# Kernel tuning notes

Hardware: AMD Instinct MI355X
Metric: run time of the kernel (lower is better)

The kernel has to match this reference:

```python
import jax, jax.numpy as jnp
import numpy as np

B, L, DEPTH, W = 32, 256, 4, 32

def setup_inputs() -> dict:
    key = jax.random.key(0)
    ks = jax.random.split(key, 12)
    rn = lambda k, sh: jax.random.normal(k, sh, dtype=jnp.float32)
    return {
        "x": rn(ks[0], (B, L, L)),
        "ai": rn(ks[1], (W, 1)),
        "ao": rn(ks[2], (1, W)),
        "a": rn(ks[3], (DEPTH, W, W)),
        "bi": rn(ks[4], (W, 1)),
        "bo": rn(ks[5], (1, W)),
        "b": rn(ks[6], (DEPTH, W, W)),
        "ci": rn(ks[7], (W, 1)),
        "co": rn(ks[8], (1, W)),
        "c": rn(ks[9], (DEPTH, W, W)),
        "bias_i": rn(ks[10], (W,)),
        "bias": rn(ks[11], (DEPTH, W)),
    }

def _layer(x, wc, wb, wa, bias):
    # x: [b, ci, X, Y]; wc/wb/wa: [co, ci]; circular 3x3 stencil via rolls
    y = jnp.einsum('oi,bixy->boxy', wc, x)
    nb = (jnp.roll(x, 1, axis=2) + jnp.roll(x, -1, axis=2)
          + jnp.roll(x, 1, axis=3) + jnp.roll(x, -1, axis=3))
    y = y + jnp.einsum('oi,bixy->boxy', wb, nb)
    dg = (jnp.roll(x, (1, 1), axis=(2, 3)) + jnp.roll(x, (-1, -1), axis=(2, 3))
          + jnp.roll(x, (1, -1), axis=(2, 3)) + jnp.roll(x, (-1, 1), axis=(2, 3)))
    y = y + jnp.einsum('oi,bixy->boxy', wa, dg)
    if bias is not None:
        y = y + bias[None, :, None, None]
    return y

def _act(x):
    # torch nn.GELU() default is exact (erf-based)
    return jax.nn.gelu(x, approximate=False)

def _func(x, ai, ao, a, bi, bo, b, ci, co, c, bias_i, bias):
    h = x[:, None, :, :]                       # [b,1,L,L]
    h = _act(_layer(h, ci, bi, ai, bias_i))    # [b,W,L,L]
    for k in range(a.shape[0]):
        h = _act(_layer(h, c[k], b[k], a[k], bias[k]))
    y = _layer(h, co, bo, ao, None)            # [b,1,L,L]
    return jnp.squeeze(y, axis=1)              # [b,L,L]

def reference(x, ai, ao, a, bi, bo, b, ci, co, c, bias_i, bias):
    f = lambda v: _func(v, ai, ao, a, bi, bo, b, ci, co, c, bias_i, bias)
    return 0.5 * (f(x) - f(-x))
```

## Files before the change

### kernel.cpp

```cpp
#include <hip/hip_runtime.h>
#include <hip/hip_bf16.h>

#define B_ 32
#define L_ 256
#define W_ 32
#define TILE 16
#define PSTR 40
#define LL (L_*L_)

typedef float    floatx4 __attribute__((ext_vector_type(4)));
typedef float    floatx2 __attribute__((ext_vector_type(2)));
typedef short    shortx8 __attribute__((ext_vector_type(8)));
typedef unsigned uintx2  __attribute__((ext_vector_type(2)));
typedef unsigned uintx4  __attribute__((ext_vector_type(4)));

typedef const __attribute__((address_space(1))) unsigned guint_t;
typedef __attribute__((address_space(3))) unsigned luint_t;

__device__ __forceinline__ void lds_dma16(const unsigned short* src, unsigned short* dst) {
    __builtin_amdgcn_global_load_lds((guint_t*)src, (luint_t*)dst, 16, 0, 0);
}

__device__ __forceinline__ floatx2 fma2(floatx2 a, floatx2 b, floatx2 c) {
#if __has_builtin(__builtin_elementwise_fma)
    return __builtin_elementwise_fma(a, b, c);
#else
    return floatx2{fmaf(a.x, b.x, c.x), fmaf(a.y, b.y, c.y)};
#endif
}

#if __has_builtin(__builtin_amdgcn_cvt_pk_bf16_f32)
__device__ __forceinline__ unsigned pack_bf2(float a, float b) {
    auto v = __builtin_amdgcn_cvt_pk_bf16_f32(a, b);
    return __builtin_bit_cast(unsigned, v);
}
#else
__device__ __forceinline__ unsigned pack_bf2(float a, float b) {
    unsigned ua = __float_as_uint(a);
    unsigned ub = __float_as_uint(b);
    ua += 0x7fffu + ((ua >> 16) & 1u);
    ub += 0x7fffu + ((ub >> 16) & 1u);
    return (ua >> 16) | (ub & 0xffff0000u);
}
#endif

__device__ __forceinline__ unsigned gelu2_pack(floatx2 x) {
    floatx2 x2    = x * x;
    floatx2 t     = x2 * 0.044715f;
    floatx2 inner = fma2(t, x, x);
    floatx2 z     = inner * -2.3022082299446597f;
    float e0 = __builtin_amdgcn_exp2f(z.x);
    float e1 = __builtin_amdgcn_exp2f(z.y);
    float r0 = __builtin_amdgcn_rcpf(1.0f + e0);
    float r1 = __builtin_amdgcn_rcpf(1.0f + e1);
    floatx2 g = x * floatx2{r0, r1};
    return pack_bf2(g.x, g.y);
}

__device__ __forceinline__ int swizzle_blk(int p) {
    return (p & 7) * 1024 + (p >> 3);
}

__device__ __forceinline__ void conv9(
        const shortx8& t00, const shortx8& t01, const shortx8& t02,
        const shortx8& t10, const shortx8& t11, const shortx8& t12,
        const shortx8& t20, const shortx8& t21, const shortx8& t22,
        const shortx8 af[3][2], const floatx4 bvv[2], floatx4 acc[2]) {
    #pragma unroll
    for (int h = 0; h < 2; ++h) {
        acc[h] = __builtin_amdgcn_mfma_f32_16x16x32_bf16(af[0][h], t11, bvv[h], 0, 0, 0);
        acc[h] = __builtin_amdgcn_mfma_f32_16x16x32_bf16(af[1][h], t01, acc[h], 0, 0, 0);
        acc[h] = __builtin_amdgcn_mfma_f32_16x16x32_bf16(af[1][h], t21, acc[h], 0, 0, 0);
        acc[h] = __builtin_amdgcn_mfma_f32_16x16x32_bf16(af[1][h], t10, acc[h], 0, 0, 0);
        acc[h] = __builtin_amdgcn_mfma_f32_16x16x32_bf16(af[1][h], t12, acc[h], 0, 0, 0);
        acc[h] = __builtin_amdgcn_mfma_f32_16x16x32_bf16(af[2][h], t00, acc[h], 0, 0, 0);
        acc[h] = __builtin_amdgcn_mfma_f32_16x16x32_bf16(af[2][h], t02, acc[h], 0, 0, 0);
        acc[h] = __builtin_amdgcn_mfma_f32_16x16x32_bf16(af[2][h], t20, acc[h], 0, 0, 0);
        acc[h] = __builtin_amdgcn_mfma_f32_16x16x32_bf16(af[2][h], t22, acc[h], 0, 0, 0);
    }
}

__device__ __forceinline__ void conv9x2(
        const shortx8 r0[3], const shortx8 r1[3],
        const shortx8 r2[3], const shortx8 r3[3],
        const shortx8 af[3][2], const floatx4 bvv[2],
        floatx4 accA[2], floatx4 accB[2]) {
    const shortx8* ra[3] = { r0, r1, r2 };
    const shortx8* rb[3] = { r1, r2, r3 };
    const int F[9] = {0,1,1,1,1,2,2,2,2};
    const int R[9] = {1,0,2,1,1,0,0,2,2};
    const int C[9] = {1,1,1,0,2,0,2,0,2};
    #pragma unroll
    for (int k = 0; k < 9; ++k)
      #pragma unroll
      for (int h = 0; h < 2; ++h) {
        accA[h] = __builtin_amdgcn_mfma_f32_16x16x32_bf16(af[F[k]][h], ra[R[k]][C[k]],
                      (k == 0) ? bvv[h] : accA[h], 0, 0, 0);
        accB[h] = __builtin_amdgcn_mfma_f32_16x16x32_bf16(af[F[k]][h], rb[R[k]][C[k]],
                      (k == 0) ? bvv[h] : accB[h], 0, 0, 0);
      }
}

__device__ __forceinline__ void conv9x2_last(
        const shortx8 r0[3], const shortx8 r1[3],
        const shortx8 r2[3], const shortx8 r3[3],
        const shortx8 afl[3], const floatx4& zc, floatx4& accA, floatx4& accB) {
    const shortx8* ra[3] = { r0, r1, r2 };
    const shortx8* rb[3] = { r1, r2, r3 };
    const int F[9] = {0,1,1,1,1,2,2,2,2};
    const int R[9] = {1,0,2,1,1,0,0,2,2};
    const int C[9] = {1,1,1,0,2,0,2,0,2};
    #pragma unroll
    for (int k = 0; k < 9; ++k) {
        accA = __builtin_amdgcn_mfma_f32_16x16x32_bf16(afl[F[k]], ra[R[k]][C[k]],
                   (k == 0) ? zc : accA, 0, 0, 0);
        accB = __builtin_amdgcn_mfma_f32_16x16x32_bf16(afl[F[k]], rb[R[k]][C[k]],
                   (k == 0) ? zc : accB, 0, 0, 0);
    }
}

__device__ __forceinline__ void gelu_pack4(const floatx4 acc[2], unsigned d[4]) {
    d[0] = gelu2_pack(floatx2{acc[0][0], acc[0][1]});
    d[1] = gelu2_pack(floatx2{acc[0][2], acc[0][3]});
    d[2] = gelu2_pack(floatx2{acc[1][0], acc[1][1]});
    d[3] = gelu2_pack(floatx2{acc[1][2], acc[1][3]});
}

__device__ __forceinline__ void build_afrag(
        const float* wc, const float* wb, const float* wa, const float* bias,
        int m, int q, shortx8 af[3][2], floatx4 bvv[2]) {
    const float* wm[3] = { wc, wb, wa };
    #pragma unroll
    for (int f = 0; f < 3; ++f)
      #pragma unroll
      for (int h = 0; h < 2; ++h) {
        const float* row = wm[f] + (h*16 + m) * W_ + q*8;
        floatx4 r0 = *(const floatx4*)(row);
        floatx4 r1 = *(const floatx4*)(row + 4);
        union { shortx8 s; unsigned u[4]; } w;
        w.u[0] = pack_bf2(r0.x, r0.y);
        w.u[1] = pack_bf2(r0.z, r0.w);
        w.u[2] = pack_bf2(r1.x, r1.y);
        w.u[3] = pack_bf2(r1.z, r1.w);
        af[f][h] = w.s;
      }
    #pragma unroll
    for (int h = 0; h < 2; ++h)
        bvv[h] = *(const floatx4*)(bias + h*16 + q*4);
}

__global__ __launch_bounds__(256) void kern_first(
        const float* __restrict__ x, float scale,
        const float* __restrict__ ci, const float* __restrict__ bi,
        const float* __restrict__ ai, const float* __restrict__ bias_i,
        unsigned short* __restrict__ hout) {
    __shared__ float tile[18*18];
    __shared__ float wC[W_], wB[W_], wA[W_], bs[W_];
    int blk = swizzle_blk(blockIdx.x);
    int b = blk >> 8;
    int t = blk & 255;
    int x0 = (t >> 4) * TILE;
    int y0 = (t & 15) * TILE;
    int tid = threadIdx.x;
    if (tid < W_) { wC[tid] = ci[tid]; wB[tid] = bi[tid]; wA[tid] = ai[tid]; bs[tid] = bias_i[tid]; }
    const float* xb = x + (size_t)b * LL;
    for (int idx = tid; idx < 18*18; idx += 256) {
        int dy = idx / 18, dx = idx % 18;
        int gx = (x0 + dy - 1) & 255;
        int gy = (y0 + dx - 1) & 255;
        tile[idx] = scale * xb[gx * L_ + gy];
    }
    __syncthreads();
    int dx = tid & 15, dy = tid >> 4;
    const float* c0 = &tile[dy * 18 + dx];
    float ctr = c0[19];
    float nb  = c0[1] + c0[37] + c0[18] + c0[20];
    float dg  = c0[0] + c0[2] + c0[36] + c0[38];
    floatx2 ctr2 = floatx2{ctr, ctr};
    floatx2 nb2  = floatx2{nb, nb};
    floatx2 dg2  = floatx2{dg, dg};
    unsigned od[16];
    #pragma unroll
    for (int o = 0; o < 16; ++o) {
        floatx2 wcv = *(const floatx2*)(&wC[2*o]);
        floatx2 wbv = *(const floatx2*)(&wB[2*o]);
        floatx2 wav = *(const floatx2*)(&wA[2*o]);
        floatx2 bsv = *(const floatx2*)(&bs[2*o]);
        floatx2 v = fma2(wcv, ctr2, fma2(wbv, nb2, fma2(wav, dg2, bsv)));
        od[o] = gelu2_pack(v);
    }
    unsigned* dst = (unsigned*)(hout + (((((size_t)b << 8) | (unsigned)(x0+dy)) << 8 | (unsigned)(y0+dx)) << 5));
    *(uintx4*)(dst)      = uintx4{od[0],  od[1],  od[2],  od[3]};
    *(uintx4*)(dst + 4)  = uintx4{od[4],  od[5],  od[6],  od[7]};
    *(uintx4*)(dst + 8)  = uintx4{od[8],  od[9],  od[10], od[11]};
    *(uintx4*)(dst + 12) = uintx4{od[12], od[13], od[14], od[15]};
}

__global__ __launch_bounds__(256, 4) void kern_mid2(
        const unsigned short* __restrict__ hin,
        const float* __restrict__ wc1, const float* __restrict__ wb1,
        const float* __restrict__ wa1, const float* __restrict__ bias1,
        const float* __restrict__ wc2, const float* __restrict__ wb2,
        const float* __restrict__ wa2, const float* __restrict__ bias2,
        unsigned short* __restrict__ hout) {
    __shared__ unsigned short tile2[400 * PSTR];

    const int tid = threadIdx.x;
    const int blk = swizzle_blk(blockIdx.x);
    const int b  = blk >> 8;
    const int t  = blk & 255;
    const int x0 = (t >> 4) * TILE;
    const int y0 = (t & 15) * TILE;

    const unsigned short* hb = hin + ((size_t)b << 21);

    #pragma unroll
    for (int jj = 0; jj < 8; ++jj) {
        int j = tid + jj * 256;
        if (j < 2000) {
            int pos = (j * 3277) >> 14;
            int qtr = j - pos * 5;
            int qe  = qtr < 4 ? qtr : 3;
            int r = (pos * 3277) >> 16;
            int c = pos - r * 20;
            int gx = (x0 + r - 2) & 255;
            int gy = (y0 + c - 2) & 255;
            const unsigned short* src = hb + ((((unsigned)gx << 8) | (unsigned)gy) << 5) + qe*8;
            lds_dma16(src, tile2 + (size_t)j * 8);
        }
    }

    const int lane = tid & 63;
    const int wv   = tid >> 6;
    const int m    = lane & 15;
    const int q    = lane >> 4;

    shortx8 afrag[3][2];
    floatx4 bvv[2];
    build_afrag(wc1, wb1, wa1, bias1, m, q, afrag, bvv);

    __syncthreads();

#define LDT(tr, off) (*(const shortx8*)(tile2 + (((tr)*20 + m + (off)))*PSTR + q*8))

    const int trow0 = wv * 4;
    shortx8 R0[3], R1[3], R2[3], R3[3], R4[3], R5[3];
    #pragma unroll
    for (int o = 0; o < 3; ++o) {
        R0[o] = LDT(trow0 + 0, o);
        R1[o] = LDT(trow0 + 1, o);
        R2[o] = LDT(trow0 + 2, o);
        R3[o] = LDT(trow0 + 3, o);
    }
    unsigned heldA[2][4];
    {
        floatx4 accA[2], accB[2];
        conv9x2(R0, R1, R2, R3, afrag, bvv, accA, accB);
        gelu_pack4(accA, heldA[0]);
        gelu_pack4(accB, heldA[1]);
    }
    #pragma unroll
    for (int o = 0; o < 3; ++o) {
        R4[o] = LDT(trow0 + 4, o);
        R5[o] = LDT(trow0 + 5, o);
    }
    {
        floatx4 accA[2], accB[2];
        conv9x2(R2, R3, R4, R5, afrag, bvv, accA, accB);
        unsigned dA[4], dB[4];
        gelu_pack4(accA, dA);
        gelu_pack4(accB, dB);
        unsigned short* wpA = tile2 + ((trow0 + 2)*20 + m)*PSTR + q*4;
        *(uintx2*)(wpA)      = uintx2{dA[0], dA[1]};
        *(uintx2*)(wpA + 16) = uintx2{dA[2], dA[3]};
        unsigned short* wpB = tile2 + ((trow0 + 3)*20 + m)*PSTR + q*4;
        *(uintx2*)(wpB)      = uintx2{dB[0], dB[1]};
        *(uintx2*)(wpB + 16) = uintx2{dB[2], dB[3]};
    }

    int er0, ec0;
    if (wv == 0)      { er0 = 16; ec0 = m;  }
    else if (wv == 1) { er0 = 17; ec0 = m;  }
    else if (wv == 2) { er0 = m;  ec0 = 16; }
    else              { er0 = m;  ec0 = 17; }
    unsigned heldE[4];
    {
        shortx8 T[3][3];
        #pragma unroll
        for (int i = 0; i < 3; ++i)
          #pragma unroll
          for (int o = 0; o < 3; ++o)
            T[i][o] = *(const shortx8*)(tile2 + ((er0 + i)*20 + ec0 + o)*PSTR + q*8);
        floatx4 acc[2];
        conv9(T[0][0], T[0][1], T[0][2], T[1][0], T[1][1], T[1][2],
              T[2][0], T[2][1], T[2][2], afrag, bvv, acc);
        gelu_pack4(acc, heldE);
    }
    const int heldEoff = (er0*20 + ec0)*PSTR + q*4;

    unsigned heldC[4];
    int heldCoff = 0;
    if (wv == 2) {
        int sr = 16 + ((m >> 1) & 1);
        int sc = 16 + (m & 1);
        shortx8 T[3][3];
        #pragma unroll
        for (int i = 0; i < 3; ++i)
          #pragma unroll
          for (int o = 0; o < 3; ++o)
            T[i][o] = *(const shortx8*)(tile2 + ((sr + i)*20 + sc + o)*PSTR + q*8);
        floatx4 acc[2];
        conv9(T[0][0], T[0][1], T[0][2], T[1][0], T[1][1], T[1][2],
              T[2][0], T[2][1], T[2][2], afrag, bvv, acc);
        gelu_pack4(acc, heldC);
        heldCoff = (sr*20 + sc)*PSTR + q*4;
    }

    __syncthreads();

    #pragma unroll
    for (int rr = 0; rr < 2; ++rr) {
        unsigned short* wp = tile2 + ((trow0 + rr)*20 + m)*PSTR + q*4;
        *(uintx2*)(wp)      = uintx2{heldA[rr][0], heldA[rr][1]};
        *(uintx2*)(wp + 16) = uintx2{heldA[rr][2], heldA[rr][3]};
    }
    {
        unsigned short* wp = tile2 + heldEoff;
        *(uintx2*)(wp)      = uintx2{heldE[0], heldE[1]};
        *(uintx2*)(wp + 16) = uintx2{heldE[2], heldE[3]};
    }
    if (wv == 2 && m < 4) {
        unsigned short* wp = tile2 + heldCoff;
        *(uintx2*)(wp)      = uintx2{heldC[0], heldC[1]};
        *(uintx2*)(wp + 16) = uintx2{heldC[2], heldC[3]};
    }

    build_afrag(wc2, wb2, wa2, bias2, m, q, afrag, bvv);

    __syncthreads();

    unsigned short* outb = hout + ((size_t)b << 21);
    #pragma unroll
    for (int o = 0; o < 3; ++o) {
        R0[o] = LDT(trow0 + 0, o);
        R1[o] = LDT(trow0 + 1, o);
        R2[o] = LDT(trow0 + 2, o);
        R3[o] = LDT(trow0 + 3, o);
    }
    {
        floatx4 accA[2], accB[2];
        conv9x2(R0, R1, R2, R3, afrag, bvv, accA, accB);
        unsigned dA[4], dB[4];
        gelu_pack4(accA, dA);
        gelu_pack4(accB, dB);
        unsigned short* dstA = outb + ((((unsigned)(x0 + trow0 + 0) << 8) | (unsigned)(y0 + m)) << 5) + q*4;
        *(uintx2*)(dstA)      = uintx2{dA[0], dA[1]};
        *(uintx2*)(dstA + 16) = uintx2{dA[2], dA[3]};
        unsigned short* dstB = outb + ((((unsigned)(x0 + trow0 + 1) << 8) | (unsigned)(y0 + m)) << 5) + q*4;
        *(uintx2*)(dstB)      = uintx2{dB[0], dB[1]};
        *(uintx2*)(dstB + 16) = uintx2{dB[2], dB[3]};
    }
    #pragma unroll
    for (int o = 0; o < 3; ++o) {
        R4[o] = LDT(trow0 + 4, o);
        R5[o] = LDT(trow0 + 5, o);
    }
    {
        floatx4 accA[2], accB[2];
        conv9x2(R2, R3, R4, R5, afrag, bvv, accA, accB);
        unsigned dA[4], dB[4];
        gelu_pack4(accA, dA);
        gelu_pack4(accB, dB);
        unsigned short* dstA = outb + ((((unsigned)(x0 + trow0 + 2) << 8) | (unsigned)(y0 + m)) << 5) + q*4;
        *(uintx2*)(dstA)      = uintx2{dA[0], dA[1]};
        *(uintx2*)(dstA + 16) = uintx2{dA[2], dA[3]};
        unsigned short* dstB = outb + ((((unsigned)(x0 + trow0 + 3) << 8) | (unsigned)(y0 + m)) << 5) + q*4;
        *(uintx2*)(dstB)      = uintx2{dB[0], dB[1]};
        *(uintx2*)(dstB + 16) = uintx2{dB[2], dB[3]};
    }
#undef LDT
}

__global__ __launch_bounds__(256, 6) void kern_last(
        const unsigned short* __restrict__ hin,
        const float* __restrict__ co, const float* __restrict__ bo,
        const float* __restrict__ ao,
        float* __restrict__ out, int mode) {
    __shared__ unsigned short tile2[324 * PSTR];
    const int tid = threadIdx.x;
    const int blk = swizzle_blk(blockIdx.x);
    const int b  = blk >> 8;
    const int t  = blk & 255;
    const int x0 = (t >> 4) * TILE;
    const int y0 = (t & 15) * TILE;

    const unsigned short* hb = hin + ((size_t)b << 21);
    #pragma unroll
    for (int jj = 0; jj < 7; ++jj) {
        int j = tid + jj * 256;
        if (j < 1620) {
            int pos = (j * 3277) >> 14;
            int qtr = j - pos * 5;
            int qe  = qtr < 4 ? qtr : 3;
            int r = (pos * 3641) >> 16;
            int c = pos - r * 18;
            int gx = (x0 + r - 1) & 255;
            int gy = (y0 + c - 1) & 255;
            const unsigned short* src = hb + ((((unsigned)gx << 8) | (unsigned)gy) << 5) + qe*8;
            lds_dma16(src, tile2 + (size_t)j * 8);
        }
    }

    const int lane = tid & 63;
    const int wv   = tid >> 6;
    const int m    = lane & 15;
    const int q    = lane >> 4;

    const float* wm[3] = { co, bo, ao };
    shortx8 afl[3];
    float z = (m == 0) ? 1.0f : 0.0f;
    #pragma unroll
    for (int f = 0; f < 3; ++f) {
        const float* row = wm[f] + q*8;
        floatx4 r0 = *(const floatx4*)(row);
        floatx4 r1 = *(const floatx4*)(row + 4);
        union { shortx8 s; unsigned u[4]; } w;
        w.u[0] = pack_bf2(r0.x * z, r0.y * z);
        w.u[1] = pack_bf2(r0.z * z, r0.w * z);
        w.u[2] = pack_bf2(r1.x * z, r1.y * z);
        w.u[3] = pack_bf2(r1.z * z, r1.w * z);
        afl[f] = w.s;
    }
    const floatx4 zc = {0.f, 0.f, 0.f, 0.f};

    __syncthreads();

#define LDT18(tr, off) (*(const shortx8*)(tile2 + (((tr)*18 + m + (off)))*PSTR + q*8))
    const int trow0 = wv * 4;
    shortx8 R0[3], R1[3], R2[3], R3[3], R4[3], R5[3];
    #pragma unroll
    for (int o = 0; o < 3; ++o) {
        R0[o] = LDT18(trow0 + 0, o);
        R1[o] = LDT18(trow0 + 1, o);
        R2[o] = LDT18(trow0 + 2, o);
        R3[o] = LDT18(trow0 + 3, o);
    }
    {
        floatx4 aA, aB;
        conv9x2_last(R0, R1, R2, R3, afl, zc, aA, aB);
        if (q == 0) {
            size_t o0 = (size_t)b * LL + (size_t)(x0 + trow0 + 0) * L_ + (y0 + m);
            size_t o1 = (size_t)b * LL + (size_t)(x0 + trow0 + 1) * L_ + (y0 + m);
            float v0 = 0.5f * aA[0];
            float v1 = 0.5f * aB[0];
            if (mode == 0) { out[o0] = v0;           out[o1] = v1;           }
            else           { out[o0] = out[o0] - v0; out[o1] = out[o1] - v1; }
        }
    }
    #pragma unroll
    for (int o = 0; o < 3; ++o) {
        R4[o] = LDT18(trow0 + 4, o);
        R5[o] = LDT18(trow0 + 5, o);
    }
    {
        floatx4 aA, aB;
        conv9x2_last(R2, R3, R4, R5, afl, zc, aA, aB);
        if (q == 0) {
            size_t o0 = (size_t)b * LL + (size_t)(x0 + trow0 + 2) * L_ + (y0 + m);
            size_t o1 = (size_t)b * LL + (size_t)(x0 + trow0 + 3) * L_ + (y0 + m);
            float v0 = 0.5f * aA[0];
            float v1 = 0.5f * aB[0];
            if (mode == 0) { out[o0] = v0;           out[o1] = v1;           }
            else           { out[o0] = out[o0] - v0; out[o1] = out[o1] - v1; }
        }
    }
#undef LDT18
}

extern "C" void kernel_launch(void* const* d_in, const int* in_sizes, int n_in,
                              void* d_out, int out_size, void* d_ws, size_t ws_size,
                              hipStream_t stream) {
    const float* x      = (const float*)d_in[0];
    const float* ai     = (const float*)d_in[1];
    const float* ao     = (const float*)d_in[2];
    const float* a      = (const float*)d_in[3];
    const float* bi     = (const float*)d_in[4];
    const float* bo     = (const float*)d_in[5];
    const float* b      = (const float*)d_in[6];
    const float* ci     = (const float*)d_in[7];
    const float* co     = (const float*)d_in[8];
    const float* c      = (const float*)d_in[9];
    const float* bias_i = (const float*)d_in[10];
    const float* bias   = (const float*)d_in[11];
    float* out = (float*)d_out;

    const size_t elems = (size_t)B_ * W_ * LL;
    unsigned short* hA = (unsigned short*)d_ws;
    unsigned short* hB = hA + elems;

    dim3 grid(B_ * 256), blk(256);
    const int WW = W_ * W_;
    for (int s = 0; s < 2; ++s) {
        float scale = s ? -1.0f : 1.0f;
        kern_first<<<grid, blk, 0, stream>>>(x, scale, ci, bi, ai, bias_i, hA);
        kern_mid2<<<grid, blk, 0, stream>>>(hA,
            c, b, a, bias,
            c + WW, b + WW, a + WW, bias + W_,
            hB);
        kern_mid2<<<grid, blk, 0, stream>>>(hB,
            c + 2*WW, b + 2*WW, a + 2*WW, bias + 2*W_,
            c + 3*WW, b + 3*WW, a + 3*WW, bias + 3*W_,
            hA);
        kern_last<<<grid, blk, 0, stream>>>(hA, co, bo, ao, out, s);
    }
}
```

Baseline: 721.0 us.

## Fuse first pointwise layer with the first two stencil layers in one kernel

The first 1-channel stencil layer is now computed inside a new fused kernel that builds a 20x20 halo tile of layer-0 activations in LDS from a 22x22 input patch, then runs two MFMA stencil layers as kern_mid2 did. This removes one full-size bf16 activation write and read through global memory and one kernel launch per sign pass. In exchange each block recomputes the halo ring of layer 0 and uses more LDS, which may reduce occupancy.

```diff
diff --git a/kernel.cpp b/kernel.cpp
--- a/kernel.cpp
+++ b/kernel.cpp
@@ -7,6 +7,7 @@
 #define TILE 16
 #define PSTR 40
 #define LL (L_*L_)
+#define ELEMS ((size_t)B_ * W_ * LL)
 
 typedef float    floatx4 __attribute__((ext_vector_type(4)));
 typedef float    floatx2 __attribute__((ext_vector_type(2)));
@@ -43,6 +44,13 @@
     return (ua >> 16) | (ub & 0xffff0000u);
 }
 #endif
+
+__device__ __forceinline__ float gelu_fast(float x) {
+    float x2 = x * x;
+    float inner = fmaf(0.044715f * x2, x, x);
+    float e = __builtin_amdgcn_exp2f(inner * -2.3022082299446597f);
+    return x * __builtin_amdgcn_rcpf(1.0f + e);
+}
 
 __device__ __forceinline__ unsigned gelu2_pack(floatx2 x) {
     floatx2 x2    = x * x;
@@ -61,14 +69,15 @@
     return (p & 7) * 1024 + (p >> 3);
 }
 
-__device__ __forceinline__ void conv9(
+__device__ __forceinline__ void conv9_v1(
         const shortx8& t00, const shortx8& t01, const shortx8& t02,
         const shortx8& t10, const shortx8& t11, const shortx8& t12,
         const shortx8& t20, const shortx8& t21, const shortx8& t22,
-        const shortx8 af[3][2], const floatx4 bvv[2], floatx4 acc[2]) {
+        const shortx8 af[3][2], const float bv[2][4], floatx4 acc[2]) {
     #pragma unroll
     for (int h = 0; h < 2; ++h) {
-        acc[h] = __builtin_amdgcn_mfma_f32_16x16x32_bf16(af[0][h], t11, bvv[h], 0, 0, 0);
+        acc[h] = floatx4{bv[h][0], bv[h][1], bv[h][2], bv[h][3]};
+        acc[h] = __builtin_amdgcn_mfma_f32_16x16x32_bf16(af[0][h], t11, acc[h], 0, 0, 0);
         acc[h] = __builtin_amdgcn_mfma_f32_16x16x32_bf16(af[1][h], t01, acc[h], 0, 0, 0);
         acc[h] = __builtin_amdgcn_mfma_f32_16x16x32_bf16(af[1][h], t21, acc[h], 0, 0, 0);
         acc[h] = __builtin_amdgcn_mfma_f32_16x16x32_bf16(af[1][h], t10, acc[h], 0, 0, 0);
@@ -80,55 +89,16 @@
     }
 }
 
-__device__ __forceinline__ void conv9x2(
-        const shortx8 r0[3], const shortx8 r1[3],
-        const shortx8 r2[3], const shortx8 r3[3],
-        const shortx8 af[3][2], const floatx4 bvv[2],
-        floatx4 accA[2], floatx4 accB[2]) {
-    const shortx8* ra[3] = { r0, r1, r2 };
-    const shortx8* rb[3] = { r1, r2, r3 };
-    const int F[9] = {0,1,1,1,1,2,2,2,2};
-    const int R[9] = {1,0,2,1,1,0,0,2,2};
-    const int C[9] = {1,1,1,0,2,0,2,0,2};
-    #pragma unroll
-    for (int k = 0; k < 9; ++k)
-      #pragma unroll
-      for (int h = 0; h < 2; ++h) {
-        accA[h] = __builtin_amdgcn_mfma_f32_16x16x32_bf16(af[F[k]][h], ra[R[k]][C[k]],
-                      (k == 0) ? bvv[h] : accA[h], 0, 0, 0);
-        accB[h] = __builtin_amdgcn_mfma_f32_16x16x32_bf16(af[F[k]][h], rb[R[k]][C[k]],
-                      (k == 0) ? bvv[h] : accB[h], 0, 0, 0);
-      }
-}
-
-__device__ __forceinline__ void conv9x2_last(
-        const shortx8 r0[3], const shortx8 r1[3],
-        const shortx8 r2[3], const shortx8 r3[3],
-        const shortx8 afl[3], const floatx4& zc, floatx4& accA, floatx4& accB) {
-    const shortx8* ra[3] = { r0, r1, r2 };
-    const shortx8* rb[3] = { r1, r2, r3 };
-    const int F[9] = {0,1,1,1,1,2,2,2,2};
-    const int R[9] = {1,0,2,1,1,0,0,2,2};
-    const int C[9] = {1,1,1,0,2,0,2,0,2};
-    #pragma unroll
-    for (int k = 0; k < 9; ++k) {
-        accA = __builtin_amdgcn_mfma_f32_16x16x32_bf16(afl[F[k]], ra[R[k]][C[k]],
-                   (k == 0) ? zc : accA, 0, 0, 0);
-        accB = __builtin_amdgcn_mfma_f32_16x16x32_bf16(afl[F[k]], rb[R[k]][C[k]],
-                   (k == 0) ? zc : accB, 0, 0, 0);
-    }
-}
-
-__device__ __forceinline__ void gelu_pack4(const floatx4 acc[2], unsigned d[4]) {
-    d[0] = gelu2_pack(floatx2{acc[0][0], acc[0][1]});
-    d[1] = gelu2_pack(floatx2{acc[0][2], acc[0][3]});
-    d[2] = gelu2_pack(floatx2{acc[1][0], acc[1][1]});
-    d[3] = gelu2_pack(floatx2{acc[1][2], acc[1][3]});
-}
-
-__device__ __forceinline__ void build_afrag(
+__device__ __forceinline__ void gelu_pack4_v1(const floatx4 acc[2], unsigned d[4]) {
+    d[0] = pack_bf2(gelu_fast(acc[0][0]), gelu_fast(acc[0][1]));
+    d[1] = pack_bf2(gelu_fast(acc[0][2]), gelu_fast(acc[0][3]));
+    d[2] = pack_bf2(gelu_fast(acc[1][0]), gelu_fast(acc[1][1]));
+    d[3] = pack_bf2(gelu_fast(acc[1][2]), gelu_fast(acc[1][3]));
+}
+
+__device__ __forceinline__ void build_afrag_v1(
         const float* wc, const float* wb, const float* wa, const float* bias,
-        int m, int q, shortx8 af[3][2], floatx4 bvv[2]) {
+        int m, int q, shortx8 af[3][2], float bv[2][4]) {
     const float* wm[3] = { wc, wb, wa };
     #pragma unroll
     for (int f = 0; f < 3; ++f)
@@ -146,54 +116,293 @@
       }
     #pragma unroll
     for (int h = 0; h < 2; ++h)
+      #pragma unroll
+      for (int r = 0; r < 4; ++r)
+        bv[h][r] = bias[h*16 + q*4 + r];
+}
+
+__device__ __forceinline__ void conv9(
+        const shortx8& t00, const shortx8& t01, const shortx8& t02,
+        const shortx8& t10, const shortx8& t11, const shortx8& t12,
+        const shortx8& t20, const shortx8& t21, const shortx8& t22,
+        const shortx8 af[3][2], const floatx4 bvv[2], floatx4 acc[2]) {
+    #pragma unroll
+    for (int h = 0; h < 2; ++h) {
+        acc[h] = __builtin_amdgcn_mfma_f32_16x16x32_bf16(af[0][h], t11, bvv[h], 0, 0, 0);
+        acc[h] = __builtin_amdgcn_mfma_f32_16x16x32_bf16(af[1][h], t01, acc[h], 0, 0, 0);
+        acc[h] = __builtin_amdgcn_mfma_f32_16x16x32_bf16(af[1][h], t21, acc[h], 0, 0, 0);
+        acc[h] = __builtin_amdgcn_mfma_f32_16x16x32_bf16(af[1][h], t10, acc[h], 0, 0, 0);
+        acc[h] = __builtin_amdgcn_mfma_f32_16x16x32_bf16(af[1][h], t12, acc[h], 0, 0, 0);
+        acc[h] = __builtin_amdgcn_mfma_f32_16x16x32_bf16(af[2][h], t00, acc[h], 0, 0, 0);
+        acc[h] = __builtin_amdgcn_mfma_f32_16x16x32_bf16(af[2][h], t02, acc[h], 0, 0, 0);
+        acc[h] = __builtin_amdgcn_mfma_f32_16x16x32_bf16(af[2][h], t20, acc[h], 0, 0, 0);
+        acc[h] = __builtin_amdgcn_mfma_f32_16x16x32_bf16(af[2][h], t22, acc[h], 0, 0, 0);
+    }
+}
+
+__device__ __forceinline__ void conv9x2(
+        const shortx8 r0[3], const shortx8 r1[3],
+        const shortx8 r2[3], const shortx8 r3[3],
+        const shortx8 af[3][2], const floatx4 bvv[2],
+        floatx4 accA[2], floatx4 accB[2]) {
+    const shortx8* ra[3] = { r0, r1, r2 };
+    const shortx8* rb[3] = { r1, r2, r3 };
+    const int F[9] = {0,1,1,1,1,2,2,2,2};
+    const int R[9] = {1,0,2,1,1,0,0,2,2};
+    const int C[9] = {1,1,1,0,2,0,2,0,2};
+    #pragma unroll
+    for (int k = 0; k < 9; ++k)
+      #pragma unroll
+      for (int h = 0; h < 2; ++h) {
+        accA[h] = __builtin_amdgcn_mfma_f32_16x16x32_bf16(af[F[k]][h], ra[R[k]][C[k]],
+                      (k == 0) ? bvv[h] : accA[h], 0, 0, 0);
+        accB[h] = __builtin_amdgcn_mfma_f32_16x16x32_bf16(af[F[k]][h], rb[R[k]][C[k]],
+                      (k == 0) ? bvv[h] : accB[h], 0, 0, 0);
+      }
+}
+
+__device__ __forceinline__ void conv9x2_last(
+        const shortx8 r0[3], const shortx8 r1[3],
+        const shortx8 r2[3], const shortx8 r3[3],
+        const shortx8 afl[3], const floatx4& zc, floatx4& accA, floatx4& accB) {
+    const shortx8* ra[3] = { r0, r1, r2 };
+    const shortx8* rb[3] = { r1, r2, r3 };
+    const int F[9] = {0,1,1,1,1,2,2,2,2};
+    const int R[9] = {1,0,2,1,1,0,0,2,2};
+    const int C[9] = {1,1,1,0,2,0,2,0,2};
+    #pragma unroll
+    for (int k = 0; k < 9; ++k) {
+        accA = __builtin_amdgcn_mfma_f32_16x16x32_bf16(afl[F[k]], ra[R[k]][C[k]],
+                   (k == 0) ? zc : accA, 0, 0, 0);
+        accB = __builtin_amdgcn_mfma_f32_16x16x32_bf16(afl[F[k]], rb[R[k]][C[k]],
+                   (k == 0) ? zc : accB, 0, 0, 0);
+    }
+}
+
+__device__ __forceinline__ void gelu_pack4(const floatx4 acc[2], unsigned d[4]) {
+    d[0] = gelu2_pack(floatx2{acc[0][0], acc[0][1]});
+    d[1] = gelu2_pack(floatx2{acc[0][2], acc[0][3]});
+    d[2] = gelu2_pack(floatx2{acc[1][0], acc[1][1]});
+    d[3] = gelu2_pack(floatx2{acc[1][2], acc[1][3]});
+}
+
+__device__ __forceinline__ void build_afrag(
+        const float* wc, const float* wb, const float* wa, const float* bias,
+        int m, int q, shortx8 af[3][2], floatx4 bvv[2]) {
+    const float* wm[3] = { wc, wb, wa };
+    #pragma unroll
+    for (int f = 0; f < 3; ++f)
+      #pragma unroll
+      for (int h = 0; h < 2; ++h) {
+        const float* row = wm[f] + (h*16 + m) * W_ + q*8;
+        floatx4 r0 = *(const floatx4*)(row);
+        floatx4 r1 = *(const floatx4*)(row + 4);
+        union { shortx8 s; unsigned u[4]; } w;
+        w.u[0] = pack_bf2(r0.x, r0.y);
+        w.u[1] = pack_bf2(r0.z, r0.w);
+        w.u[2] = pack_bf2(r1.x, r1.y);
+        w.u[3] = pack_bf2(r1.z, r1.w);
+        af[f][h] = w.s;
+      }
+    #pragma unroll
+    for (int h = 0; h < 2; ++h)
         bvv[h] = *(const floatx4*)(bias + h*16 + q*4);
 }
 
-__global__ __launch_bounds__(256) void kern_first(
+__global__ __launch_bounds__(256, 4) void kern_front(
         const float* __restrict__ x, float scale,
         const float* __restrict__ ci, const float* __restrict__ bi,
         const float* __restrict__ ai, const float* __restrict__ bias_i,
+        const float* __restrict__ wc1, const float* __restrict__ wb1,
+        const float* __restrict__ wa1, const float* __restrict__ bias1,
+        const float* __restrict__ wc2, const float* __restrict__ wb2,
+        const float* __restrict__ wa2, const float* __restrict__ bias2,
         unsigned short* __restrict__ hout) {
-    __shared__ float tile[18*18];
+    __shared__ unsigned short tile2[400 * PSTR];
+    __shared__ float xs[22 * 23];
     __shared__ float wC[W_], wB[W_], wA[W_], bs[W_];
-    int blk = swizzle_blk(blockIdx.x);
-    int b = blk >> 8;
-    int t = blk & 255;
-    int x0 = (t >> 4) * TILE;
-    int y0 = (t & 15) * TILE;
-    int tid = threadIdx.x;
+
+    const int tid = threadIdx.x;
+    const int blk = swizzle_blk(blockIdx.x);
+    const int b  = blk >> 8;
+    const int t  = blk & 255;
+    const int x0 = (t >> 4) * TILE;
+    const int y0 = (t & 15) * TILE;
+
     if (tid < W_) { wC[tid] = ci[tid]; wB[tid] = bi[tid]; wA[tid] = ai[tid]; bs[tid] = bias_i[tid]; }
+
     const float* xb = x + (size_t)b * LL;
-    for (int idx = tid; idx < 18*18; idx += 256) {
-        int dy = idx / 18, dx = idx % 18;
-        int gx = (x0 + dy - 1) & 255;
-        int gy = (y0 + dx - 1) & 255;
-        tile[idx] = scale * xb[gx * L_ + gy];
+    #pragma unroll
+    for (int ss = 0; ss < 2; ++ss) {
+        int idx = tid + ss * 256;
+        if (idx < 484) {
+            int r = (idx * 2979) >> 16;
+            int c = idx - r * 22;
+            int gx = (x0 + r - 3) & 255;
+            int gy = (y0 + c - 3) & 255;
+            xs[r * 23 + c] = scale * xb[gx * L_ + gy];
+        }
     }
     __syncthreads();
-    int dx = tid & 15, dy = tid >> 4;
-    const float* c0 = &tile[dy * 18 + dx];
-    float ctr = c0[19];
-    float nb  = c0[1] + c0[37] + c0[18] + c0[20];
-    float dg  = c0[0] + c0[2] + c0[36] + c0[38];
-    floatx2 ctr2 = floatx2{ctr, ctr};
-    floatx2 nb2  = floatx2{nb, nb};
-    floatx2 dg2  = floatx2{dg, dg};
-    unsigned od[16];
-    #pragma unroll
-    for (int o = 0; o < 16; ++o) {
-        floatx2 wcv = *(const floatx2*)(&wC[2*o]);
-        floatx2 wbv = *(const floatx2*)(&wB[2*o]);
-        floatx2 wav = *(const floatx2*)(&wA[2*o]);
-        floatx2 bsv = *(const floatx2*)(&bs[2*o]);
-        floatx2 v = fma2(wcv, ctr2, fma2(wbv, nb2, fma2(wav, dg2, bsv)));
-        od[o] = gelu2_pack(v);
-    }
-    unsigned* dst = (unsigned*)(hout + (((((size_t)b << 8) | (unsigned)(x0+dy)) << 8 | (unsigned)(y0+dx)) << 5));
-    *(uintx4*)(dst)      = uintx4{od[0],  od[1],  od[2],  od[3]};
-    *(uintx4*)(dst + 4)  = uintx4{od[4],  od[5],  od[6],  od[7]};
-    *(uintx4*)(dst + 8)  = uintx4{od[8],  od[9],  od[10], od[11]};
-    *(uintx4*)(dst + 12) = uintx4{od[12], od[13], od[14], od[15]};
+
+    #pragma unroll
+    for (int ss = 0; ss < 2; ++ss) {
+        int idx = tid + ss * 256;
+        if (idx < 400) {
+            int i = (idx * 3277) >> 16;
+            int j = idx - i * 20;
+            const float* p0 = &xs[i * 23 + j];
+            float ctr = p0[24];
+            float nb  = p0[1] + p0[47] + p0[23] + p0[25];
+            float dg  = p0[0] + p0[2] + p0[46] + p0[48];
+            unsigned od[16];
+            #pragma unroll
+            for (int o = 0; o < 16; ++o) {
+                float v0 = gelu_fast(wC[2*o]*ctr + wB[2*o]*nb + wA[2*o]*dg + bs[2*o]);
+                float v1 = gelu_fast(wC[2*o+1]*ctr + wB[2*o+1]*nb + wA[2*o+1]*dg + bs[2*o+1]);
+                od[o] = pack_bf2(v0, v1);
+            }
+            unsigned* dst = (unsigned*)(tile2 + idx * PSTR);
+            *(uintx4*)(dst)      = uintx4{od[0],  od[1],  od[2],  od[3]};
+            *(uintx4*)(dst + 4)  = uintx4{od[4],  od[5],  od[6],  od[7]};
+            *(uintx4*)(dst + 8)  = uintx4{od[8],  od[9],  od[10], od[11]};
+            *(uintx4*)(dst + 12) = uintx4{od[12], od[13], od[14], od[15]};
+        }
+    }
+
+    const int lane = tid & 63;
+    const int wv   = tid >> 6;
+    const int m    = lane & 15;
+    const int q    = lane >> 4;
+
+    shortx8 afrag[3][2];
+    float bv[2][4];
+    build_afrag_v1(wc1, wb1, wa1, bias1, m, q, afrag, bv);
+
+    __syncthreads();
+
+#define LDT(tr, off) (*(const shortx8*)(tile2 + (((tr)*20 + m + (off)))*PSTR + q*8))
+
+    const int trow0 = wv * 4;
+    shortx8 W[3][3];
+    #pragma unroll
+    for (int i = 0; i < 3; ++i) {
+        W[i][0] = LDT(trow0 + i, 0);
+        W[i][1] = LDT(trow0 + i, 1);
+        W[i][2] = LDT(trow0 + i, 2);
+    }
+    unsigned heldA[2][4];
+    #pragma unroll
+    for (int rr = 0; rr < 4; ++rr) {
+        const int top = rr % 3, mid = (rr + 1) % 3, bot = (rr + 2) % 3;
+        floatx4 acc[2];
+        conv9_v1(W[top][0], W[top][1], W[top][2],
+                 W[mid][0], W[mid][1], W[mid][2],
+                 W[bot][0], W[bot][1], W[bot][2], afrag, bv, acc);
+        unsigned d[4];
+        gelu_pack4_v1(acc, d);
+        if (rr < 2) {
+            heldA[rr][0] = d[0]; heldA[rr][1] = d[1];
+            heldA[rr][2] = d[2]; heldA[rr][3] = d[3];
+        } else {
+            unsigned short* wp = tile2 + ((trow0 + rr)*20 + m)*PSTR + q*4;
+            *(uintx2*)(wp)      = uintx2{d[0], d[1]};
+            *(uintx2*)(wp + 16) = uintx2{d[2], d[3]};
+        }
+        if (rr < 3) {
+            W[top][0] = LDT(trow0 + rr + 3, 0);
+            W[top][1] = LDT(trow0 + rr + 3, 1);
+            W[top][2] = LDT(trow0 + rr + 3, 2);
+        }
+    }
+
+    int er0, ec0;
+    if (wv == 0)      { er0 = 16; ec0 = m;  }
+    else if (wv == 1) { er0 = 17; ec0 = m;  }
+    else if (wv == 2) { er0 = m;  ec0 = 16; }
+    else              { er0 = m;  ec0 = 17; }
+    unsigned heldE[4];
+    {
+        shortx8 T[3][3];
+        #pragma unroll
+        for (int i = 0; i < 3; ++i)
+          #pragma unroll
+          for (int o = 0; o < 3; ++o)
+            T[i][o] = *(const shortx8*)(tile2 + ((er0 + i)*20 + ec0 + o)*PSTR + q*8);
+        floatx4 acc[2];
+        conv9_v1(T[0][0], T[0][1], T[0][2], T[1][0], T[1][1], T[1][2],
+                 T[2][0], T[2][1], T[2][2], afrag, bv, acc);
+        gelu_pack4_v1(acc, heldE);
+    }
+    const int heldEoff = (er0*20 + ec0)*PSTR + q*4;
+
+    unsigned heldC[4];
+    int heldCoff = 0;
+    if (wv == 2) {
+        int sr = 16 + ((m >> 1) & 1);
+        int sc = 16 + (m & 1);
+        shortx8 T[3][3];
+        #pragma unroll
+        for (int i = 0; i < 3; ++i)
+          #pragma unroll
+          for (int o = 0; o < 3; ++o)
+            T[i][o] = *(const shortx8*)(tile2 + ((sr + i)*20 + sc + o)*PSTR + q*8);
+        floatx4 acc[2];
+        conv9_v1(T[0][0], T[0][1], T[0][2], T[1][0], T[1][1], T[1][2],
+                 T[2][0], T[2][1], T[2][2], afrag, bv, acc);
+        gelu_pack4_v1(acc, heldC);
+        heldCoff = (sr*20 + sc)*PSTR + q*4;
+    }
+
+    __syncthreads();
+
+    #pragma unroll
+    for (int rr = 0; rr < 2; ++rr) {
+        unsigned short* wp = tile2 + ((trow0 + rr)*20 + m)*PSTR + q*4;
+        *(uintx2*)(wp)      = uintx2{heldA[rr][0], heldA[rr][1]};
+        *(uintx2*)(wp + 16) = uintx2{heldA[rr][2], heldA[rr][3]};
+    }
+    {
+        unsigned short* wp = tile2 + heldEoff;
+        *(uintx2*)(wp)      = uintx2{heldE[0], heldE[1]};
+        *(uintx2*)(wp + 16) = uintx2{heldE[2], heldE[3]};
+    }
+    if (wv == 2 && m < 4) {
+        unsigned short* wp = tile2 + heldCoff;
+        *(uintx2*)(wp)      = uintx2{heldC[0], heldC[1]};
+        *(uintx2*)(wp + 16) = uintx2{heldC[2], heldC[3]};
+    }
+
+    build_afrag_v1(wc2, wb2, wa2, bias2, m, q, afrag, bv);
+
+    __syncthreads();
+
+    unsigned short* outb = hout + ((size_t)b << 21);
+    #pragma unroll
+    for (int i = 0; i < 3; ++i) {
+        W[i][0] = LDT(trow0 + i, 0);
+        W[i][1] = LDT(trow0 + i, 1);
+        W[i][2] = LDT(trow0 + i, 2);
+    }
+    #pragma unroll
+    for (int rr = 0; rr < 4; ++rr) {
+        const int top = rr % 3, mid = (rr + 1) % 3, bot = (rr + 2) % 3;
+        floatx4 acc[2];
+        conv9_v1(W[top][0], W[top][1], W[top][2],
+                 W[mid][0], W[mid][1], W[mid][2],
+                 W[bot][0], W[bot][1], W[bot][2], afrag, bv, acc);
+        unsigned d[4];
+        gelu_pack4_v1(acc, d);
+        unsigned short* dst = outb + ((((unsigned)(x0 + trow0 + rr) << 8) | (unsigned)(y0 + m)) << 5) + q*4;
+        *(uintx2*)(dst)      = uintx2{d[0], d[1]};
+        *(uintx2*)(dst + 16) = uintx2{d[2], d[3]};
+        if (rr < 3) {
+            W[top][0] = LDT(trow0 + rr + 3, 0);
+            W[top][1] = LDT(trow0 + rr + 3, 1);
+            W[top][2] = LDT(trow0 + rr + 3, 2);
+        }
+    }
+#undef LDT
 }
 
 __global__ __launch_bounds__(256, 4) void kern_mid2(
@@ -494,16 +703,15 @@
     const float* bias   = (const float*)d_in[11];
     float* out = (float*)d_out;
 
-    const size_t elems = (size_t)B_ * W_ * LL;
     unsigned short* hA = (unsigned short*)d_ws;
-    unsigned short* hB = hA + elems;
+    unsigned short* hB = hA + ELEMS;
 
     dim3 grid(B_ * 256), blk(256);
     const int WW = W_ * W_;
     for (int s = 0; s < 2; ++s) {
         float scale = s ? -1.0f : 1.0f;
-        kern_first<<<grid, blk, 0, stream>>>(x, scale, ci, bi, ai, bias_i, hA);
-        kern_mid2<<<grid, blk, 0, stream>>>(hA,
+        kern_front<<<grid, blk, 0, stream>>>(x, scale,
+            ci, bi, ai, bias_i,
             c, b, a, bias,
             c + WW, b + WW, a + WW, bias + W_,
             hB);
```

Measured after the change: 703.4 us (median of 2 runs). 2.4% less time.
